# Optimization experiments

Hardware: AMD Instinct MI355X
Metric: run time of the kernel (lower is better)

## Reference

```python
import jax, jax.numpy as jnp
import numpy as np

C_IN = 2048
N_EXP = 64
TOPK = 2


def setup_inputs() -> dict:
    key = jax.random.key(0)
    kx, kw, kb = jax.random.split(key, 3)
    x = jax.random.normal(kx, (4, 4096, C_IN), dtype=jnp.float32)
    # nn.Linear(c_in, n_exp): weight [n_exp, c_in], bias [n_exp]
    bound = 1.0 / np.sqrt(C_IN)
    W = jax.random.uniform(kw, (N_EXP, C_IN), minval=-bound, maxval=bound, dtype=jnp.float32)
    b = jax.random.uniform(kb, (N_EXP,), minval=-bound, maxval=bound, dtype=jnp.float32)
    return {"x": x, "W": W, "b": b}


def reference(x, W, b):
    # linear: [B,S,C] @ [C,E] + [E] -> [B,S,E]
    logits = jnp.einsum("bsc,ec->bse", x, W) + b
    probs = jax.nn.softmax(logits, axis=-1)
    vals, idx = jax.lax.top_k(probs, TOPK)  # [B,S,K]
    # scatter top-k values back to full expert dim; other entries zero
    onehot = jax.nn.one_hot(idx, N_EXP, dtype=probs.dtype)  # [B,S,K,E]
    gate_out = jnp.einsum("bsk,bske->bse", vals, onehot)
    return gate_out
```

## Files before the change

### kernel.cpp

```cpp
#include <hip/hip_runtime.h>
#include <math.h>

#define C_IN 2048
#define N_EXP 64
#define TPB 32
#define CHUNK 64
#define KWIN 512
#define NCHUNK 8
#define DELTA  3e-4f
#define DELTA2 1e-3f

typedef __bf16 bf16x8 __attribute__((ext_vector_type(8)));
typedef float f32x4 __attribute__((ext_vector_type(4)));

__device__ __forceinline__ void cvt_split(float f, ushort& h, ushort& l) {
    uint u = __float_as_uint(f);
    uint hr = (u + (0x7FFFu + ((u >> 16) & 1u))) >> 16;
    h = (ushort)hr;
    float hf = __uint_as_float(hr << 16);
    uint v = __float_as_uint(f - hf);
    l = (ushort)((v + (0x7FFFu + ((v >> 16) & 1u))) >> 16);
}

__global__ void conv_w_kernel(const float* __restrict__ W,
                              ushort* __restrict__ whf, ushort* __restrict__ wlf) {
    const int o = blockIdx.x * 256 + threadIdx.x;
    const int egks = o >> 9;
    const int lane = (o >> 3) & 63;
    const int j = o & 7;
    const int e = (egks >> 6) * 16 + (lane & 15);
    const int k = (egks & 63) * 32 + (lane >> 4) * 8 + j;
    ushort h, lo;
    cvt_split(W[e * C_IN + k], h, lo);
    whf[o] = h;
    wlf[o] = lo;
}

__global__ __launch_bounds__(256, 2) void topk_gate_kernel(
    const float* __restrict__ x, const float* __restrict__ Wf,
    const float* __restrict__ b, const ushort* __restrict__ whf,
    const ushort* __restrict__ wlf, float* __restrict__ out)
{
    __shared__ __align__(16) ushort lds[4][4096];

    const int tid = threadIdx.x;
    const int wv = tid >> 6, l = tid & 63;
    const int t0 = blockIdx.x * TPB;
    const int row_l = l >> 4;
    const int kc = l & 15;

    ushort* hbuf = lds[wv];
    ushort* lbuf = lds[wv] + 2048;

    const float* xg = x + (size_t)t0 * C_IN + wv * KWIN;

    int xwoff[8];
#pragma unroll
    for (int m = 0; m < 8; ++m)
        xwoff[m] = (m * 4 + row_l) * 64 + ((kc * 4) ^ (row_l * 16));

    int aoff[2][2];
#pragma unroll
    for (int mf = 0; mf < 2; ++mf)
#pragma unroll
    for (int ks = 0; ks < 2; ++ks) {
        const int ar = mf * 16 + (l & 15);
        aoff[mf][ks] = ar * 64 + ((ks * 32 + (l >> 4) * 8) ^ ((ar & 3) * 16));
    }

    f32x4 acc[2][4];
#pragma unroll
    for (int mf = 0; mf < 2; ++mf)
#pragma unroll
    for (int eg = 0; eg < 4; ++eg)
        acc[mf][eg] = (f32x4){0.f, 0.f, 0.f, 0.f};

    float4 xvA[8], xvB[8];
    uint4 wWA[8], wWB[8];

    auto LOADX = [&](float4* dst, int c) {
#pragma unroll
        for (int m = 0; m < 8; ++m)
            dst[m] = *(const float4*)(xg + (size_t)(m * 4 + row_l) * C_IN + c * CHUNK + kc * 4);
    };
    auto LOADW = [&](uint4* dst, int c, int ks) {
        const int ksa = wv * 16 + c * 2 + ks;
#pragma unroll
        for (int eg = 0; eg < 4; ++eg) {
            const int base = (eg * 64 + ksa) * 512 + l * 8;
            dst[eg * 2 + 0] = *(const uint4*)&whf[base];
            dst[eg * 2 + 1] = *(const uint4*)&wlf[base];
        }
    };
    auto CVTWR = [&](const float4* src) {
#pragma unroll
        for (int m = 0; m < 8; ++m) {
            ushort h0, h1, h2, h3, q0, q1, q2, q3;
            cvt_split(src[m].x, h0, q0); cvt_split(src[m].y, h1, q1);
            cvt_split(src[m].z, h2, q2); cvt_split(src[m].w, h3, q3);
            uint2 hv = {(uint)h0 | ((uint)h1 << 16), (uint)h2 | ((uint)h3 << 16)};
            uint2 lv = {(uint)q0 | ((uint)q1 << 16), (uint)q2 | ((uint)q3 << 16)};
            *(uint2*)&hbuf[xwoff[m]] = hv;
            *(uint2*)&lbuf[xwoff[m]] = lv;
        }
    };
    auto FRAGMFMA = [&](int ks, const uint4* wbuf) {
#pragma unroll
        for (int mf = 0; mf < 2; ++mf) {
            bf16x8 ah = __builtin_bit_cast(bf16x8, *(const uint4*)&hbuf[aoff[mf][ks]]);
            bf16x8 al = __builtin_bit_cast(bf16x8, *(const uint4*)&lbuf[aoff[mf][ks]]);
#pragma unroll
            for (int eg = 0; eg < 4; ++eg) {
                bf16x8 bh = __builtin_bit_cast(bf16x8, wbuf[eg * 2 + 0]);
                bf16x8 bl = __builtin_bit_cast(bf16x8, wbuf[eg * 2 + 1]);
                acc[mf][eg] = __builtin_amdgcn_mfma_f32_16x16x32_bf16(ah, bh, acc[mf][eg], 0, 0, 0);
                acc[mf][eg] = __builtin_amdgcn_mfma_f32_16x16x32_bf16(al, bh, acc[mf][eg], 0, 0, 0);
                acc[mf][eg] = __builtin_amdgcn_mfma_f32_16x16x32_bf16(ah, bl, acc[mf][eg], 0, 0, 0);
            }
        }
    };

    LOADX(xvA, 0);
    LOADX(xvB, 1);
    LOADW(wWA, 0, 0);

#pragma unroll
    for (int cc = 0; cc < NCHUNK; cc += 2) {
        LOADW(wWB, cc, 1);
        CVTWR(xvA);
        if (cc + 2 < NCHUNK) LOADX(xvA, cc + 2);
        FRAGMFMA(0, wWA);
        LOADW(wWA, cc + 1, 0);
        FRAGMFMA(1, wWB);
        LOADW(wWB, cc + 1, 1);
        CVTWR(xvB);
        if (cc + 3 < NCHUNK) LOADX(xvB, cc + 3);
        FRAGMFMA(0, wWA);
        if (cc + 2 < NCHUNK) LOADW(wWA, cc + 2, 0);
        FRAGMFMA(1, wWB);
    }

    float* fb = (float*)lds[wv];
#pragma unroll
    for (int mf = 0; mf < 2; ++mf)
#pragma unroll
    for (int eg = 0; eg < 4; ++eg)
#pragma unroll
    for (int r = 0; r < 4; ++r)
        fb[(mf * 16 + (l >> 4) * 4 + r) * 64 + eg * 16 + (l & 15)] = acc[mf][eg][r];

    __syncthreads();

    const float* f0 = (const float*)lds[0];
    const float* f1 = (const float*)lds[1];
    const float* f2 = (const float*)lds[2];
    const float* f3 = (const float*)lds[3];
    const int e = l;
    const float be = b[e];

    for (int ti = 0; ti < 8; ++ti) {
        const int t = wv * 8 + ti;
        float logit = f0[t * 64 + e] + f1[t * 64 + e]
                    + f2[t * 64 + e] + f3[t * 64 + e] + be;

        float v1, v2, v3; int i1, i2;
        for (int pass = 0; pass < 2; ++pass) {
            v1 = logit; i1 = e;
#pragma unroll
            for (int off = 32; off >= 1; off >>= 1) {
                float ov = __shfl_xor(v1, off, 64);
                int   oi = __shfl_xor(i1, off, 64);
                if (ov > v1 || (ov == v1 && oi < i1)) { v1 = ov; i1 = oi; }
            }
            v2 = (e == i1) ? -3.4e38f : logit;
            i2 = (e == i1) ? N_EXP : e;
#pragma unroll
            for (int off = 32; off >= 1; off >>= 1) {
                float ov = __shfl_xor(v2, off, 64);
                int   oi = __shfl_xor(i2, off, 64);
                if (ov > v2 || (ov == v2 && oi < i2)) { v2 = ov; i2 = oi; }
            }
            v3 = (e == i1 || e == i2) ? -3.4e38f : logit;
#pragma unroll
            for (int off = 32; off >= 1; off >>= 1) {
                float ov = __shfl_xor(v3, off, 64);
                v3 = (ov > v3) ? ov : v3;
            }
            if (pass == 1) break;
            const bool risky = (v1 - v2 < DELTA) || (v2 - v3 < DELTA);
            if (!risky) break;
            unsigned long long cm = __ballot(logit >= v2 - DELTA2);
            const float* xr = x + (size_t)(t0 + t) * C_IN;
            while (cm) {
                const int ce = __ffsll((unsigned long long)cm) - 1;
                cm &= cm - 1;
                const float* wr = Wf + (size_t)ce * C_IN;
                float p = 0.f;
#pragma unroll 8
                for (int i = 0; i < 32; ++i)
                    p = fmaf(xr[l + 64 * i], wr[l + 64 * i], p);
#pragma unroll
                for (int off = 32; off >= 1; off >>= 1)
                    p += __shfl_xor(p, off, 64);
                if (e == ce) logit = p + be;
            }
        }

        float ex = expf(logit - v1);
        float ssum = ex;
#pragma unroll
        for (int off = 32; off >= 1; off >>= 1)
            ssum += __shfl_xor(ssum, off, 64);
        const float inv = 1.0f / ssum;
        const float p1 = inv;
        const float p2 = expf(v2 - v1) * inv;
        const float o = (e == i1) ? p1 : ((e == i2) ? p2 : 0.0f);
        out[(size_t)(t0 + t) * N_EXP + e] = o;
    }
}

extern "C" void kernel_launch(void* const* d_in, const int* in_sizes, int n_in,
                              void* d_out, int out_size, void* d_ws, size_t ws_size,
                              hipStream_t stream) {
    const float* x = (const float*)d_in[0];
    const float* W = (const float*)d_in[1];
    const float* b = (const float*)d_in[2];
    float* out = (float*)d_out;

    ushort* whf = (ushort*)d_ws;
    ushort* wlf = whf + N_EXP * C_IN;

    conv_w_kernel<<<512, 256, 0, stream>>>(W, whf, wlf);

    const int tokens = in_sizes[0] / C_IN;
    const int grid = tokens / TPB;
    topk_gate_kernel<<<grid, 256, 0, stream>>>(x, W, b, whf, wlf, out);
}
```

Before: 56.73 us.

## Halve tokens per block and load x fragments directly into MFMA registers

```diff
diff --git a/kernel.cpp b/kernel.cpp
--- a/kernel.cpp
+++ b/kernel.cpp
@@ -3,10 +3,9 @@
 
 #define C_IN 2048
 #define N_EXP 64
-#define TPB 32
-#define CHUNK 64
+#define TPB 16
 #define KWIN 512
-#define NCHUNK 8
+#define KSTEPS 16
 #define DELTA  3e-4f
 #define DELTA2 1e-3f
 
@@ -36,132 +35,70 @@
     wlf[o] = lo;
 }
 
-__global__ __launch_bounds__(256, 2) void topk_gate_kernel(
+__global__ __launch_bounds__(256, 4) void topk_gate_kernel(
     const float* __restrict__ x, const float* __restrict__ Wf,
     const float* __restrict__ b, const ushort* __restrict__ whf,
     const ushort* __restrict__ wlf, float* __restrict__ out)
 {
-    __shared__ __align__(16) ushort lds[4][4096];
+    __shared__ float part[4][TPB][65];
 
     const int tid = threadIdx.x;
     const int wv = tid >> 6, l = tid & 63;
     const int t0 = blockIdx.x * TPB;
-    const int row_l = l >> 4;
-    const int kc = l & 15;
+    const int tr = l & 15;
+    const int kg = l >> 4;
 
-    ushort* hbuf = lds[wv];
-    ushort* lbuf = lds[wv] + 2048;
+    const float* xg = x + (size_t)(t0 + tr) * C_IN + wv * KWIN + kg * 8;
 
-    const float* xg = x + (size_t)t0 * C_IN + wv * KWIN;
+    f32x4 acc[4];
+#pragma unroll
+    for (int eg = 0; eg < 4; ++eg) acc[eg] = (f32x4){0.f, 0.f, 0.f, 0.f};
 
-    int xwoff[8];
+#pragma unroll 2
+    for (int ks = 0; ks < KSTEPS; ++ks) {
+        const float4 a0 = *(const float4*)(xg + ks * 32);
+        const float4 a1 = *(const float4*)(xg + ks * 32 + 4);
+        const int ksa = wv * KSTEPS + ks;
+        uint4 wb[8];
 #pragma unroll
-    for (int m = 0; m < 8; ++m)
-        xwoff[m] = (m * 4 + row_l) * 64 + ((kc * 4) ^ (row_l * 16));
-
-    int aoff[2][2];
+        for (int eg = 0; eg < 4; ++eg) {
+            wb[eg * 2 + 0] = *(const uint4*)&whf[(eg * 64 + ksa) * 512 + l * 8];
+            wb[eg * 2 + 1] = *(const uint4*)&wlf[(eg * 64 + ksa) * 512 + l * 8];
+        }
+        ushort h[8], q[8];
+        cvt_split(a0.x, h[0], q[0]); cvt_split(a0.y, h[1], q[1]);
+        cvt_split(a0.z, h[2], q[2]); cvt_split(a0.w, h[3], q[3]);
+        cvt_split(a1.x, h[4], q[4]); cvt_split(a1.y, h[5], q[5]);
+        cvt_split(a1.z, h[6], q[6]); cvt_split(a1.w, h[7], q[7]);
+        uint4 hv = {(uint)h[0] | ((uint)h[1] << 16), (uint)h[2] | ((uint)h[3] << 16),
+                    (uint)h[4] | ((uint)h[5] << 16), (uint)h[6] | ((uint)h[7] << 16)};
+        uint4 qv = {(uint)q[0] | ((uint)q[1] << 16), (uint)q[2] | ((uint)q[3] << 16),
+                    (uint)q[4] | ((uint)q[5] << 16), (uint)q[6] | ((uint)q[7] << 16)};
+        bf16x8 ah = __builtin_bit_cast(bf16x8, hv);
+        bf16x8 al = __builtin_bit_cast(bf16x8, qv);
 #pragma unroll
-    for (int mf = 0; mf < 2; ++mf)
-#pragma unroll
-    for (int ks = 0; ks < 2; ++ks) {
-        const int ar = mf * 16 + (l & 15);
-        aoff[mf][ks] = ar * 64 + ((ks * 32 + (l >> 4) * 8) ^ ((ar & 3) * 16));
+        for (int eg = 0; eg < 4; ++eg) {
+            bf16x8 bh = __builtin_bit_cast(bf16x8, wb[eg * 2 + 0]);
+            bf16x8 bl = __builtin_bit_cast(bf16x8, wb[eg * 2 + 1]);
+            acc[eg] = __builtin_amdgcn_mfma_f32_16x16x32_bf16(ah, bh, acc[eg], 0, 0, 0);
+            acc[eg] = __builtin_amdgcn_mfma_f32_16x16x32_bf16(al, bh, acc[eg], 0, 0, 0);
+            acc[eg] = __builtin_amdgcn_mfma_f32_16x16x32_bf16(ah, bl, acc[eg], 0, 0, 0);
+        }
     }
 
-    f32x4 acc[2][4];
-#pragma unroll
-    for (int mf = 0; mf < 2; ++mf)
-#pragma unroll
-    for (int eg = 0; eg < 4; ++eg)
-        acc[mf][eg] = (f32x4){0.f, 0.f, 0.f, 0.f};
-
-    float4 xvA[8], xvB[8];
-    uint4 wWA[8], wWB[8];
-
-    auto LOADX = [&](float4* dst, int c) {
-#pragma unroll
-        for (int m = 0; m < 8; ++m)
-            dst[m] = *(const float4*)(xg + (size_t)(m * 4 + row_l) * C_IN + c * CHUNK + kc * 4);
-    };
-    auto LOADW = [&](uint4* dst, int c, int ks) {
-        const int ksa = wv * 16 + c * 2 + ks;
-#pragma unroll
-        for (int eg = 0; eg < 4; ++eg) {
-            const int base = (eg * 64 + ksa) * 512 + l * 8;
-            dst[eg * 2 + 0] = *(const uint4*)&whf[base];
-            dst[eg * 2 + 1] = *(const uint4*)&wlf[base];
-        }
-    };
-    auto CVTWR = [&](const float4* src) {
-#pragma unroll
-        for (int m = 0; m < 8; ++m) {
-            ushort h0, h1, h2, h3, q0, q1, q2, q3;
-            cvt_split(src[m].x, h0, q0); cvt_split(src[m].y, h1, q1);
-            cvt_split(src[m].z, h2, q2); cvt_split(src[m].w, h3, q3);
-            uint2 hv = {(uint)h0 | ((uint)h1 << 16), (uint)h2 | ((uint)h3 << 16)};
-            uint2 lv = {(uint)q0 | ((uint)q1 << 16), (uint)q2 | ((uint)q3 << 16)};
-            *(uint2*)&hbuf[xwoff[m]] = hv;
-            *(uint2*)&lbuf[xwoff[m]] = lv;
-        }
-    };
-    auto FRAGMFMA = [&](int ks, const uint4* wbuf) {
-#pragma unroll
-        for (int mf = 0; mf < 2; ++mf) {
-            bf16x8 ah = __builtin_bit_cast(bf16x8, *(const uint4*)&hbuf[aoff[mf][ks]]);
-            bf16x8 al = __builtin_bit_cast(bf16x8, *(const uint4*)&lbuf[aoff[mf][ks]]);
-#pragma unroll
-            for (int eg = 0; eg < 4; ++eg) {
-                bf16x8 bh = __builtin_bit_cast(bf16x8, wbuf[eg * 2 + 0]);
-                bf16x8 bl = __builtin_bit_cast(bf16x8, wbuf[eg * 2 + 1]);
-                acc[mf][eg] = __builtin_amdgcn_mfma_f32_16x16x32_bf16(ah, bh, acc[mf][eg], 0, 0, 0);
-                acc[mf][eg] = __builtin_amdgcn_mfma_f32_16x16x32_bf16(al, bh, acc[mf][eg], 0, 0, 0);
-                acc[mf][eg] = __builtin_amdgcn_mfma_f32_16x16x32_bf16(ah, bl, acc[mf][eg], 0, 0, 0);
-            }
-        }
-    };
-
-    LOADX(xvA, 0);
-    LOADX(xvB, 1);
-    LOADW(wWA, 0, 0);
-
-#pragma unroll
-    for (int cc = 0; cc < NCHUNK; cc += 2) {
-        LOADW(wWB, cc, 1);
-        CVTWR(xvA);
-        if (cc + 2 < NCHUNK) LOADX(xvA, cc + 2);
-        FRAGMFMA(0, wWA);
-        LOADW(wWA, cc + 1, 0);
-        FRAGMFMA(1, wWB);
-        LOADW(wWB, cc + 1, 1);
-        CVTWR(xvB);
-        if (cc + 3 < NCHUNK) LOADX(xvB, cc + 3);
-        FRAGMFMA(0, wWA);
-        if (cc + 2 < NCHUNK) LOADW(wWA, cc + 2, 0);
-        FRAGMFMA(1, wWB);
-    }
-
-    float* fb = (float*)lds[wv];
-#pragma unroll
-    for (int mf = 0; mf < 2; ++mf)
 #pragma unroll
     for (int eg = 0; eg < 4; ++eg)
 #pragma unroll
     for (int r = 0; r < 4; ++r)
-        fb[(mf * 16 + (l >> 4) * 4 + r) * 64 + eg * 16 + (l & 15)] = acc[mf][eg][r];
-
+        part[wv][kg * 4 + r][eg * 16 + tr] = acc[eg][r];
     __syncthreads();
 
-    const float* f0 = (const float*)lds[0];
-    const float* f1 = (const float*)lds[1];
-    const float* f2 = (const float*)lds[2];
-    const float* f3 = (const float*)lds[3];
     const int e = l;
     const float be = b[e];
-
-    for (int ti = 0; ti < 8; ++ti) {
-        const int t = wv * 8 + ti;
-        float logit = f0[t * 64 + e] + f1[t * 64 + e]
-                    + f2[t * 64 + e] + f3[t * 64 + e] + be;
+    for (int ti = 0; ti < 4; ++ti) {
+        const int t = wv * 4 + ti;
+        float logit = part[0][t][e] + part[1][t][e]
+                    + part[2][t][e] + part[3][t][e] + be;
 
         float v1, v2, v3; int i1, i2;
         for (int pass = 0; pass < 2; ++pass) {
```

Result: no change. 56.47 us (-0.5%).
